# Performance work log

Hardware: AMD Instinct MI355X
Metric: run time of the kernel (lower is better)

## Reference

```python
import jax, jax.numpy as jnp
import numpy as np

PIXEL_DIM = 768
AGE_DIM = 128
B, N = 8, 2048


def setup_inputs() -> dict:
    key = jax.random.key(0)
    ks = jax.random.split(key, 8)
    s_p = 1.0 / np.sqrt(PIXEL_DIM)
    s_a = 1.0 / np.sqrt(AGE_DIM)
    return {
        "pixel_features": jax.random.normal(ks[0], (B, N, PIXEL_DIM), jnp.float32),
        "age_features": jax.random.normal(ks[1], (B, AGE_DIM), jnp.float32),
        # Linear weights stored as [in, out] (torch stores [out, in]; math identical)
        "Wq": jax.random.uniform(ks[2], (PIXEL_DIM, PIXEL_DIM), jnp.float32, -s_p, s_p),
        "bq": jax.random.uniform(ks[3], (PIXEL_DIM,), jnp.float32, -s_p, s_p),
        "Wk": jax.random.uniform(ks[4], (AGE_DIM, PIXEL_DIM), jnp.float32, -s_a, s_a),
        "bk": jax.random.uniform(ks[5], (PIXEL_DIM,), jnp.float32, -s_a, s_a),
        "Wv": jax.random.uniform(ks[6], (AGE_DIM, PIXEL_DIM), jnp.float32, -s_a, s_a),
        "bv": jax.random.uniform(ks[7], (PIXEL_DIM,), jnp.float32, -s_a, s_a),
    }


def reference(pixel_features, age_features, Wq, bq, Wk, bk, Wv, bv):
    b, n, d = pixel_features.shape
    scale = jnp.sqrt(jnp.asarray(d, jnp.float32))
    # age_features broadcast across the pixel dimension before K/V projection
    age_exp = jnp.broadcast_to(age_features[:, None, :], (b, n, age_features.shape[-1]))
    q = jnp.einsum("bnd,de->bne", pixel_features, Wq) + bq   # [B,N,D]
    k = jnp.einsum("bna,ad->bnd", age_exp, Wk) + bk          # [B,N,D]
    v = jnp.einsum("bna,ad->bnd", age_exp, Wv) + bv          # [B,N,D]
    scores = jnp.einsum("bnd,bmd->bnm", q, k) / scale        # [B,N,N]
    weights = jax.nn.softmax(scores, axis=-1)
    attended = jnp.einsum("bnm,bmd->bnd", weights, v)
    return attended + pixel_features
```

## Files before the change

kernel.cpp:

```cpp
#include <hip/hip_runtime.h>


#define PIXEL_DIM 768
#define AGE_DIM   128
#define BB        8
#define NN        2048

__global__ void ca_compute_vvec(const float* __restrict__ age,
                                const float* __restrict__ Wv,
                                const float* __restrict__ bv,
                                float* __restrict__ v_vec) {
    int tid = blockIdx.x * blockDim.x + threadIdx.x;
    if (tid >= BB * PIXEL_DIM) return;
    int b = tid / PIXEL_DIM;
    int d = tid - b * PIXEL_DIM;
    const float* ab = age + b * AGE_DIM;
    float sum = bv[d];
    #pragma unroll 8
    for (int a = 0; a < AGE_DIM; ++a) {
        sum = fmaf(ab[a], Wv[a * PIXEL_DIM + d], sum);
    }
    v_vec[tid] = sum;
}

__global__ void ca_add_bcast(const float4* __restrict__ pixel,
                             const float* __restrict__ v_vec,
                             float4* __restrict__ out) {
    const long total4 = (long)BB * NN * PIXEL_DIM / 4;
    long i = (long)blockIdx.x * blockDim.x + threadIdx.x;
    if (i >= total4) return;
    long e = i * 4;
    int d = (int)(e % PIXEL_DIM);
    int b = (int)(e / ((long)NN * PIXEL_DIM));
    float4 p = pixel[i];
    float4 v = *(const float4*)(v_vec + b * PIXEL_DIM + d);
    float4 r;
    r.x = p.x + v.x;
    r.y = p.y + v.y;
    r.z = p.z + v.z;
    r.w = p.w + v.w;
    out[i] = r;
}

extern "C" void kernel_launch(void* const* d_in, const int* in_sizes, int n_in,
                              void* d_out, int out_size, void* d_ws, size_t ws_size,
                              hipStream_t stream) {
    const float* pixel = (const float*)d_in[0];
    const float* age   = (const float*)d_in[1];
    const float* Wv    = (const float*)d_in[6];
    const float* bv    = (const float*)d_in[7];
    float* out   = (float*)d_out;
    float* v_vec = (float*)d_ws;

    {
        int threads = 256;
        int total = BB * PIXEL_DIM;
        int blocks = (total + threads - 1) / threads;
        ca_compute_vvec<<<blocks, threads, 0, stream>>>(age, Wv, bv, v_vec);
    }
    {
        int threads = 256;
        long total4 = (long)BB * NN * PIXEL_DIM / 4;
        int blocks = (int)((total4 + threads - 1) / threads);
        ca_add_bcast<<<blocks, threads, 0, stream>>>((const float4*)pixel, v_vec,
                                                     (float4*)out);
    }
}
```

Before: 116.7 us.

## Fuse v-vector projection into broadcast-add kernel with tiled nontemporal streaming

Merges the two kernels into one. Each block recomputes its 64-column slice of the v vector from age and Wv in shared memory, then streams a 128-row by 64-column tile of pixel features with nontemporal loads and stores. This removes a kernel launch and the workspace round-trip. In exchange the Wv projection is recomputed redundantly in every block (16 row-chunks per batch), and rows are accessed in 256-byte column segments instead of fully contiguous runs. The base already relies on softmax over identical keys collapsing to v, which is exact math rather than a hack.

```diff
diff --git a/kernel.cpp b/kernel.cpp
--- a/kernel.cpp
+++ b/kernel.cpp
@@ -5,41 +5,63 @@
 #define AGE_DIM   128
 #define BB        8
 #define NN        2048
+#define DCH       64
+#define NROWS     128
+#define NTHREADS  256
 
-__global__ void ca_compute_vvec(const float* __restrict__ age,
-                                const float* __restrict__ Wv,
-                                const float* __restrict__ bv,
-                                float* __restrict__ v_vec) {
-    int tid = blockIdx.x * blockDim.x + threadIdx.x;
-    if (tid >= BB * PIXEL_DIM) return;
-    int b = tid / PIXEL_DIM;
-    int d = tid - b * PIXEL_DIM;
-    const float* ab = age + b * AGE_DIM;
-    float sum = bv[d];
-    #pragma unroll 8
-    for (int a = 0; a < AGE_DIM; ++a) {
-        sum = fmaf(ab[a], Wv[a * PIXEL_DIM + d], sum);
+typedef float f32x4 __attribute__((ext_vector_type(4)));
+
+__global__ __launch_bounds__(NTHREADS) void ca_fused(
+    const float* __restrict__ pixel,
+    const float* __restrict__ age,
+    const float* __restrict__ Wv,
+    const float* __restrict__ bv,
+    float* __restrict__ out)
+{
+    __shared__ float s_age[AGE_DIM];
+    __shared__ float s_part[NTHREADS];
+    __shared__ float s_v[DCH];
+
+    const int t  = threadIdx.x;
+    const int nc = blockIdx.x;
+    const int dc = blockIdx.y;
+    const int b  = blockIdx.z;
+    const int d0 = dc * DCH;
+
+    if (t < AGE_DIM) s_age[t] = age[b * AGE_DIM + t];
+    __syncthreads();
+
+    {
+        const int j    = t >> 2;
+        const int part = t & 3;
+        const float* wcol = Wv + d0 + j;
+        float sum = 0.f;
+        #pragma unroll
+        for (int i = 0; i < 32; ++i) {
+            const int a = (part << 5) + i;
+            sum = fmaf(s_age[a], wcol[a * PIXEL_DIM], sum);
+        }
+        s_part[t] = sum;
     }
-    v_vec[tid] = sum;
-}
+    __syncthreads();
+    if (t < DCH) {
+        s_v[t] = bv[d0 + t]
+               + s_part[t * 4] + s_part[t * 4 + 1]
+               + s_part[t * 4 + 2] + s_part[t * 4 + 3];
+    }
+    __syncthreads();
 
-__global__ void ca_add_bcast(const float4* __restrict__ pixel,
-                             const float* __restrict__ v_vec,
-                             float4* __restrict__ out) {
-    const long total4 = (long)BB * NN * PIXEL_DIM / 4;
-    long i = (long)blockIdx.x * blockDim.x + threadIdx.x;
-    if (i >= total4) return;
-    long e = i * 4;
-    int d = (int)(e % PIXEL_DIM);
-    int b = (int)(e / ((long)NN * PIXEL_DIM));
-    float4 p = pixel[i];
-    float4 v = *(const float4*)(v_vec + b * PIXEL_DIM + d);
-    float4 r;
-    r.x = p.x + v.x;
-    r.y = p.y + v.y;
-    r.z = p.z + v.z;
-    r.w = p.w + v.w;
-    out[i] = r;
+    const int col = t & 15;
+    const int r0  = t >> 4;
+    const f32x4 v = *(const f32x4*)(s_v + col * 4);
+    const int base = (b * NN + nc * NROWS) * PIXEL_DIM + d0 + col * 4;
+    #pragma unroll
+    for (int k = 0; k < 8; ++k) {
+        const int idx = base + (r0 + k * 16) * PIXEL_DIM;
+        f32x4 p = __builtin_nontemporal_load((const f32x4*)(pixel + idx));
+        p += v;
+        __builtin_nontemporal_store(p, (f32x4*)(out + idx));
+    }
 }
 
 extern "C" void kernel_launch(void* const* d_in, const int* in_sizes, int n_in,
@@ -49,20 +71,8 @@
     const float* age   = (const float*)d_in[1];
     const float* Wv    = (const float*)d_in[6];
     const float* bv    = (const float*)d_in[7];
-    float* out   = (float*)d_out;
-    float* v_vec = (float*)d_ws;
+    float* out = (float*)d_out;
 
-    {
-        int threads = 256;
-        int total = BB * PIXEL_DIM;
-        int blocks = (total + threads - 1) / threads;
-        ca_compute_vvec<<<blocks, threads, 0, stream>>>(age, Wv, bv, v_vec);
-    }
-    {
-        int threads = 256;
-        long total4 = (long)BB * NN * PIXEL_DIM / 4;
-        int blocks = (int)((total4 + threads - 1) / threads);
-        ca_add_bcast<<<blocks, threads, 0, stream>>>((const float4*)pixel, v_vec,
-                                                     (float4*)out);
-    }
+    dim3 grid(NN / NROWS, PIXEL_DIM / DCH, BB);
+    ca_fused<<<grid, NTHREADS, 0, stream>>>(pixel, age, Wv, bv, out);
 }
```

Result: slower. 119.7 us (+2.6%).
